# Kernel tuning notes

Measured on AMD Instinct MI355X. Metric: run time of the kernel, lower is better.

## Reference

```python
import jax, jax.numpy as jnp
import numpy as np

VOCAB, HIDDEN, EMBED = 30522, 768, 512
PAD_INDEX = 0
NEG_SLOPE = 0.1


def setup_inputs() -> dict:
    key = jax.random.key(0)
    k1, k2, k3, k4 = jax.random.split(key, 4)
    words = jax.random.randint(k1, (16, 512, 4), 0, VOCAB, dtype=jnp.int64) if jax.config.jax_enable_x64 else jax.random.randint(k1, (16, 512, 4), 0, VOCAB, dtype=jnp.int32)
    embed_table = jax.random.normal(k2, (VOCAB, HIDDEN), dtype=jnp.float32) * 0.02
    w_ffn = jax.random.normal(k3, (HIDDEN, EMBED), dtype=jnp.float32) * 0.02
    b_ffn = jax.random.normal(k4, (EMBED,), dtype=jnp.float32) * 0.02
    return {"words": words, "embed_table": embed_table, "w_ffn": w_ffn, "b_ffn": b_ffn}


def reference(words, embed_table, w_ffn, b_ffn):
    # words: [B, S, W] subword ids; pad_index marks padding subwords/words.
    B, S, W = words.shape
    sub_mask = words != PAD_INDEX                      # [B,S,W] valid subwords
    word_valid = jnp.any(sub_mask, axis=-1)            # [B,S]  words with >=1 subword
    lens = jnp.sum(word_valid, axis=-1)                # [B]    valid words per sequence

    # Stub of transformer last_hidden_state: per-token hidden vectors. [B,S,W,H]
    x = embed_table[words]

    # Masked mean over subwords of each word (segment mean-pool).
    m = sub_mask[..., None].astype(x.dtype)
    cnt = jnp.maximum(jnp.sum(sub_mask, axis=-1), 1)[..., None].astype(x.dtype)
    pooled = jnp.sum(x * m, axis=2) / cnt              # [B,S,H]

    # pad = x[0, -1] of flattened [B, S*W, H] == hidden of last flat token of batch 0
    pad_vec = x[0, -1, -1]                             # [H]

    # Stable compaction: valid words first (mirrors pop-in-order + pad append).
    order = jnp.argsort(jnp.logical_not(word_valid), axis=1, stable=True)  # [B,S]
    pooled_c = jnp.take_along_axis(pooled, order[..., None], axis=1)       # [B,S,H]
    keep = (jnp.arange(S)[None, :] < lens[:, None])[..., None]             # [B,S,1]
    x_seq = jnp.where(keep, pooled_c, pad_vec)         # [B,S,H]

    # FFN: Linear + LeakyReLU(0.1)
    return jax.nn.leaky_relu(x_seq @ w_ffn + b_ffn, NEG_SLOPE)
```

## Files before the change

kernel.cpp:

```cpp
#include <hip/hip_runtime.h>
#include <stdint.h>

#define HIDDEN 768
#define EMBED  512
#define BATCH  16
#define SEQ    512
#define NWORDS (BATCH*SEQ)
#define PAD_FLAT_IDX 2047
#define NEG_SLOPE 0.1f
#define SA_LD 776
#define BM 32

__device__ __forceinline__ unsigned short f2bf(float f) {
    unsigned int x = __float_as_uint(f);
    unsigned int r = x + 0x7fffu + ((x >> 16) & 1u);
    return (unsigned short)(r >> 16);
}

__global__ __launch_bounds__(256) void prep_kernel(const int* __restrict__ words,
                                                   const float* __restrict__ w,
                                                   int4* __restrict__ ids4,
                                                   int* __restrict__ cnts,
                                                   unsigned short* __restrict__ wt) {
    if (blockIdx.x < BATCH) {
        int b = blockIdx.x;
        int t = threadIdx.x;
        int s0 = 2 * t, s1 = 2 * t + 1;
        int4 wa = ((const int4*)words)[b * SEQ + s0];
        int4 wb = ((const int4*)words)[b * SEQ + s1];
        bool v0 = (wa.x | wa.y | wa.z | wa.w) != 0;
        bool v1 = (wb.x | wb.y | wb.z | wb.w) != 0;

        unsigned long long m0 = __ballot(v0);
        unsigned long long m1 = __ballot(v1);
        int lane = t & 63;
        int wave = t >> 6;
        unsigned long long below = (1ull << lane) - 1ull;
        int pre = __popcll(m0 & below) + __popcll(m1 & below);
        __shared__ int wsum[4];
        if (lane == 0) wsum[wave] = __popcll(m0) + __popcll(m1);
        __syncthreads();
        int off = 0, tot = 0;
#pragma unroll
        for (int i = 0; i < 4; ++i) {
            int x = wsum[i];
            if (i < wave) off += x;
            tot += x;
        }
        int vp0 = off + pre;
        int vp1 = vp0 + (v0 ? 1 : 0);
        int d0 = v0 ? vp0 : (tot + (s0 - vp0));
        int d1 = v1 ? vp1 : (tot + (s1 - vp1));

        int pid = words[PAD_FLAT_IDX];

        {
            int id[4] = {wa.x, wa.y, wa.z, wa.w};
            int o[4] = {0, 0, 0, 0};
            int c = 0;
#pragma unroll
            for (int j = 0; j < 4; ++j) if (id[j] != 0) o[c++] = id[j];
            if (c == 0) { o[0] = pid; c = 1; }
            ids4[b * SEQ + d0] = make_int4(o[0], o[1], o[2], o[3]);
            cnts[b * SEQ + d0] = c;
        }
        {
            int id[4] = {wb.x, wb.y, wb.z, wb.w};
            int o[4] = {0, 0, 0, 0};
            int c = 0;
#pragma unroll
            for (int j = 0; j < 4; ++j) if (id[j] != 0) o[c++] = id[j];
            if (c == 0) { o[0] = pid; c = 1; }
            ids4[b * SEQ + d1] = make_int4(o[0], o[1], o[2], o[3]);
            cnts[b * SEQ + d1] = c;
        }
    } else {
        __shared__ float tile[32][33];
        int bid = blockIdx.x - BATCH;
        int k0 = (bid % (HIDDEN / 32)) * 32;
        int n0 = (bid / (HIDDEN / 32)) * 32;
        int tc = threadIdx.x & 31;
        int tr = threadIdx.x >> 5;
#pragma unroll
        for (int i = 0; i < 4; ++i) {
            int r = tr + i * 8;
            tile[r][tc] = w[(size_t)(k0 + r) * EMBED + n0 + tc];
        }
        __syncthreads();
#pragma unroll
        for (int i = 0; i < 4; ++i) {
            int r = tr + i * 8;
            wt[(size_t)(n0 + r) * HIDDEN + k0 + tc] = f2bf(tile[tc][r]);
        }
    }
}

typedef __attribute__((ext_vector_type(8))) short bf16x8;
typedef __attribute__((ext_vector_type(4))) float f32x4;

__device__ __forceinline__ void load_lds16(const void* g, void* l) {
    __builtin_amdgcn_global_load_lds(
        (const __attribute__((address_space(1))) unsigned int*)g,
        (__attribute__((address_space(3))) unsigned int*)l,
        16, 0, 0);
}

__global__ __launch_bounds__(256) void fused_kernel(const int4* __restrict__ ids4,
                                                    const int* __restrict__ cnts,
                                                    const float* __restrict__ table,
                                                    const unsigned short* __restrict__ Bt,
                                                    const float* __restrict__ bias,
                                                    float* __restrict__ out) {
    __shared__ unsigned short sA[BM * SA_LD];
    __shared__ unsigned short sB[512 * 32];

    int tid  = threadIdx.x;
    int wave = tid >> 6;
    int lane = tid & 63;
    int m0   = blockIdx.x * BM;

#pragma unroll 2
    for (int i = 0; i < 8; ++i) {
        int rl  = i * 4 + wave;
        int row = m0 + rl;
        int4 w4 = ids4[row];
        int cnt = cnts[row];
        int id[4] = {w4.x, w4.y, w4.z, w4.w};
        float sx[3] = {0.f, 0.f, 0.f}, sy[3] = {0.f, 0.f, 0.f};
        float sz[3] = {0.f, 0.f, 0.f}, sw[3] = {0.f, 0.f, 0.f};
#pragma unroll
        for (int j = 0; j < 4; ++j) {
            if (j < cnt) {
                const float4* rp = (const float4*)(table + (size_t)id[j] * HIDDEN);
#pragma unroll
                for (int c = 0; c < 3; ++c) {
                    float4 v = rp[lane + 64 * c];
                    sx[c] += v.x; sy[c] += v.y; sz[c] += v.z; sw[c] += v.w;
                }
            }
        }
        float inv = 1.0f / (float)cnt;
#pragma unroll
        for (int c = 0; c < 3; ++c) {
            ushort4 o;
            o.x = f2bf(sx[c] * inv); o.y = f2bf(sy[c] * inv);
            o.z = f2bf(sz[c] * inv); o.w = f2bf(sw[c] * inv);
            *(ushort4*)&sA[rl * SA_LD + (lane + 64 * c) * 4] = o;
        }
    }

    int quad = lane >> 4;
    int l16  = lane & 15;
    f32x4 acc[2][8] = {};

    const unsigned short* gb = Bt + (size_t)(tid >> 2) * HIDDEN + (tid & 3) * 8;

    for (int k0 = 0; k0 < HIDDEN; k0 += 32) {
#pragma unroll
        for (int j = 0; j < 8; ++j)
            load_lds16(gb + (size_t)j * 64 * HIDDEN + k0, &sB[(tid + 256 * j) * 8]);
        __syncthreads();

        bf16x8 af[2], bfr[8];
#pragma unroll
        for (int mt = 0; mt < 2; ++mt)
            af[mt] = *(const bf16x8*)&sA[(mt * 16 + l16) * SA_LD + k0 + quad * 8];
#pragma unroll
        for (int nt = 0; nt < 8; ++nt)
            bfr[nt] = *(const bf16x8*)&sB[(wave * 128 + nt * 16 + l16) * 32 + quad * 8];

#pragma unroll
        for (int mt = 0; mt < 2; ++mt)
#pragma unroll
            for (int nt = 0; nt < 8; ++nt)
                acc[mt][nt] = __builtin_amdgcn_mfma_f32_16x16x32_bf16(
                    af[mt], bfr[nt], acc[mt][nt], 0, 0, 0);
        __syncthreads();
    }

#pragma unroll
    for (int nt = 0; nt < 8; ++nt) {
        int col = wave * 128 + nt * 16 + l16;
        float bv = bias[col];
#pragma unroll
        for (int mt = 0; mt < 2; ++mt) {
            int rbase = m0 + mt * 16 + quad * 4;
#pragma unroll
            for (int r = 0; r < 4; ++r) {
                float v = acc[mt][nt][r] + bv;
                v = (v > 0.f) ? v : v * NEG_SLOPE;
                out[(size_t)(rbase + r) * EMBED + col] = v;
            }
        }
    }
}

extern "C" void kernel_launch(void* const* d_in, const int* in_sizes, int n_in,
                              void* d_out, int out_size, void* d_ws, size_t ws_size,
                              hipStream_t stream) {
    (void)in_sizes; (void)n_in; (void)out_size; (void)ws_size;
    const int*   words = (const int*)d_in[0];
    const float* table = (const float*)d_in[1];
    const float* wffn  = (const float*)d_in[2];
    const float* bffn  = (const float*)d_in[3];
    float* out = (float*)d_out;

    char* ws = (char*)d_ws;
    unsigned short* wt   = (unsigned short*)ws;
    int4*           ids4 = (int4*)(ws + 786432);
    int*            cnts = (int*)(ws + 786432 + 131072);

    prep_kernel<<<BATCH + (HIDDEN / 32) * (EMBED / 32), 256, 0, stream>>>(
        words, wffn, ids4, cnts, wt);
    fused_kernel<<<NWORDS / BM, 256, 0, stream>>>(ids4, cnts, table, wt, bffn, out);
}
```

Before: 174.2 us.

## Split fused pool+GEMM into separate pool and tiled GEMM kernels with k-major layout

The fused kernel is split in two. A pooling kernel writes bf16 pooled rows to a global k-chunk-major buffer, and a separate GEMM kernel uses 128x64 tiles over a 2D grid, loading both operands via direct global-to-LDS copies in a k-major 8-element interleaved layout. The weight transpose now emits the same k-chunk layout. This aims to raise GEMM parallelism and reuse: 512 blocks instead of 256, and each block no longer streams the whole weight matrix per 32 rows. The cost is an extra 12MB intermediate round-trip through global memory and one more kernel launch.

```diff
diff --git a/kernel.cpp b/kernel.cpp
--- a/kernel.cpp
+++ b/kernel.cpp
@@ -6,10 +6,11 @@
 #define BATCH  16
 #define SEQ    512
 #define NWORDS (BATCH*SEQ)
+#define NKC    (HIDDEN/8)
 #define PAD_FLAT_IDX 2047
 #define NEG_SLOPE 0.1f
-#define SA_LD 776
-#define BM 32
+#define SP_LD 780
+
 
 __device__ __forceinline__ unsigned short f2bf(float f) {
     unsigned int x = __float_as_uint(f);
@@ -21,7 +22,7 @@
                                                    const float* __restrict__ w,
                                                    int4* __restrict__ ids4,
                                                    int* __restrict__ cnts,
-                                                   unsigned short* __restrict__ wt) {
+                                                   unsigned short* __restrict__ wtk) {
     if (blockIdx.x < BATCH) {
         int b = blockIdx.x;
         int t = threadIdx.x;
@@ -53,7 +54,6 @@
         int d1 = v1 ? vp1 : (tot + (s1 - vp1));
 
         int pid = words[PAD_FLAT_IDX];
-
         {
             int id[4] = {wa.x, wa.y, wa.z, wa.w};
             int o[4] = {0, 0, 0, 0};
@@ -87,37 +87,25 @@
             tile[r][tc] = w[(size_t)(k0 + r) * EMBED + n0 + tc];
         }
         __syncthreads();
+        int kc = (k0 >> 3) + (tc >> 3);
+        int ko = tc & 7;
 #pragma unroll
         for (int i = 0; i < 4; ++i) {
-            int r = tr + i * 8;
-            wt[(size_t)(n0 + r) * HIDDEN + k0 + tc] = f2bf(tile[tc][r]);
-        }
-    }
-}
-
-typedef __attribute__((ext_vector_type(8))) short bf16x8;
-typedef __attribute__((ext_vector_type(4))) float f32x4;
-
-__device__ __forceinline__ void load_lds16(const void* g, void* l) {
-    __builtin_amdgcn_global_load_lds(
-        (const __attribute__((address_space(1))) unsigned int*)g,
-        (__attribute__((address_space(3))) unsigned int*)l,
-        16, 0, 0);
-}
-
-__global__ __launch_bounds__(256) void fused_kernel(const int4* __restrict__ ids4,
-                                                    const int* __restrict__ cnts,
-                                                    const float* __restrict__ table,
-                                                    const unsigned short* __restrict__ Bt,
-                                                    const float* __restrict__ bias,
-                                                    float* __restrict__ out) {
-    __shared__ unsigned short sA[BM * SA_LD];
-    __shared__ unsigned short sB[512 * 32];
-
+            int n = n0 + tr + i * 8;
+            wtk[(size_t)kc * (EMBED * 8) + n * 8 + ko] = f2bf(tile[tc][n - n0]);
+        }
+    }
+}
+
+__global__ __launch_bounds__(256) void pool_kernel(const int4* __restrict__ ids4,
+                                                   const int* __restrict__ cnts,
+                                                   const float* __restrict__ table,
+                                                   unsigned short* __restrict__ xkm) {
+    __shared__ unsigned short sp[32 * SP_LD];
     int tid  = threadIdx.x;
     int wave = tid >> 6;
     int lane = tid & 63;
-    int m0   = blockIdx.x * BM;
+    int m0   = blockIdx.x * 32;
 
 #pragma unroll 2
     for (int i = 0; i < 8; ++i) {
@@ -145,46 +133,90 @@
             ushort4 o;
             o.x = f2bf(sx[c] * inv); o.y = f2bf(sy[c] * inv);
             o.z = f2bf(sz[c] * inv); o.w = f2bf(sw[c] * inv);
-            *(ushort4*)&sA[rl * SA_LD + (lane + 64 * c) * 4] = o;
-        }
-    }
-
+            *(ushort4*)&sp[rl * SP_LD + (lane + 64 * c) * 4] = o;
+        }
+    }
+    __syncthreads();
+
+    int rw = lane & 31;
+    int hf = lane >> 5;
+    for (int kc = wave; kc < NKC; kc += 4) {
+        ushort4 v = *(const ushort4*)&sp[rw * SP_LD + kc * 8 + hf * 4];
+        *(ushort4*)&xkm[(size_t)kc * (NWORDS * 8) + (m0 + rw) * 8 + hf * 4] = v;
+    }
+}
+
+typedef __attribute__((ext_vector_type(8))) short bf16x8;
+typedef __attribute__((ext_vector_type(4))) float f32x4;
+
+__device__ __forceinline__ void load_lds16(const void* g, void* l) {
+    __builtin_amdgcn_global_load_lds(
+        (const __attribute__((address_space(1))) unsigned int*)g,
+        (__attribute__((address_space(3))) unsigned int*)l,
+        16, 0, 0);
+}
+
+#define BM 128
+#define BN 64
+#define BK 32
+
+__global__ __launch_bounds__(256) void gemm_kernel(const unsigned short* __restrict__ xkm,
+                                                   const unsigned short* __restrict__ wtk,
+                                                   const float* __restrict__ bias,
+                                                   float* __restrict__ out) {
+    __shared__ unsigned short sA[4 * BM * 8];
+    __shared__ unsigned short sB[4 * BN * 8];
+
+    int tid  = threadIdx.x;
+    int m0   = blockIdx.x * BM;
+    int n0   = blockIdx.y * BN;
+    int wave = tid >> 6;
+    int lane = tid & 63;
+    int wr   = wave >> 1;
+    int wc   = wave & 1;
     int quad = lane >> 4;
     int l16  = lane & 15;
-    f32x4 acc[2][8] = {};
-
-    const unsigned short* gb = Bt + (size_t)(tid >> 2) * HIDDEN + (tid & 3) * 8;
-
-    for (int k0 = 0; k0 < HIDDEN; k0 += 32) {
-#pragma unroll
-        for (int j = 0; j < 8; ++j)
-            load_lds16(gb + (size_t)j * 64 * HIDDEN + k0, &sB[(tid + 256 * j) * 8]);
-        __syncthreads();
-
-        bf16x8 af[2], bfr[8];
-#pragma unroll
-        for (int mt = 0; mt < 2; ++mt)
-            af[mt] = *(const bf16x8*)&sA[(mt * 16 + l16) * SA_LD + k0 + quad * 8];
-#pragma unroll
-        for (int nt = 0; nt < 8; ++nt)
-            bfr[nt] = *(const bf16x8*)&sB[(wave * 128 + nt * 16 + l16) * 32 + quad * 8];
-
-#pragma unroll
-        for (int mt = 0; mt < 2; ++mt)
-#pragma unroll
-            for (int nt = 0; nt < 8; ++nt)
+
+    f32x4 acc[4][2] = {};
+
+    const unsigned short* gA0 = xkm + (size_t)(tid >> 7) * (NWORDS * 8) + (m0 + (tid & 127)) * 8;
+    const unsigned short* gA1 = xkm + (size_t)((tid + 256) >> 7) * (NWORDS * 8) + (m0 + ((tid + 256) & 127)) * 8;
+    const unsigned short* gB  = wtk + (size_t)(tid >> 6) * (EMBED * 8) + (n0 + (tid & 63)) * 8;
+
+    for (int k0 = 0; k0 < HIDDEN; k0 += BK) {
+        load_lds16(gA0 + (size_t)k0 * (NWORDS), &sA[tid * 8]);
+        load_lds16(gA1 + (size_t)k0 * (NWORDS), &sA[(256 + tid) * 8]);
+        load_lds16(gB  + (size_t)k0 * (EMBED),  &sB[tid * 8]);
+        __syncthreads();
+
+        bf16x8 af[4], bfr[2];
+#pragma unroll
+        for (int mt = 0; mt < 4; ++mt) {
+            int row_l = wr * 64 + mt * 16 + l16;
+            af[mt] = *(const bf16x8*)&sA[(quad * BM + row_l) * 8];
+        }
+#pragma unroll
+        for (int nt = 0; nt < 2; ++nt) {
+            int col_l = wc * 32 + nt * 16 + l16;
+            bfr[nt] = *(const bf16x8*)&sB[(quad * BN + col_l) * 8];
+        }
+
+#pragma unroll
+        for (int mt = 0; mt < 4; ++mt)
+#pragma unroll
+            for (int nt = 0; nt < 2; ++nt)
                 acc[mt][nt] = __builtin_amdgcn_mfma_f32_16x16x32_bf16(
                     af[mt], bfr[nt], acc[mt][nt], 0, 0, 0);
         __syncthreads();
     }
 
 #pragma unroll
-    for (int nt = 0; nt < 8; ++nt) {
-        int col = wave * 128 + nt * 16 + l16;
+    for (int nt = 0; nt < 2; ++nt) {
+        int col = n0 + wc * 32 + nt * 16 + l16;
         float bv = bias[col];
 #pragma unroll
-        for (int mt = 0; mt < 2; ++mt) {
-            int rbase = m0 + mt * 16 + quad * 4;
+        for (int mt = 0; mt < 4; ++mt) {
+            int rbase = m0 + wr * 64 + mt * 16 + quad * 4;
 #pragma unroll
             for (int r = 0; r < 4; ++r) {
                 float v = acc[mt][nt][r] + bv;
@@ -206,11 +238,13 @@
     float* out = (float*)d_out;
 
     char* ws = (char*)d_ws;
-    unsigned short* wt   = (unsigned short*)ws;
-    int4*           ids4 = (int4*)(ws + 786432);
-    int*            cnts = (int*)(ws + 786432 + 131072);
+    unsigned short* xkm  = (unsigned short*)ws;
+    unsigned short* wtk  = (unsigned short*)(ws + 12582912);
+    int4*           ids4 = (int4*)(ws + 12582912 + 786432);
+    int*            cnts = (int*)(ws + 12582912 + 786432 + 131072);
 
     prep_kernel<<<BATCH + (HIDDEN / 32) * (EMBED / 32), 256, 0, stream>>>(
-        words, wffn, ids4, cnts, wt);
-    fused_kernel<<<NWORDS / BM, 256, 0, stream>>>(ids4, cnts, table, wt, bffn, out);
-}
+        words, wffn, ids4, cnts, wtk);
+    pool_kernel<<<NWORDS / 32, 256, 0, stream>>>(ids4, cnts, table, xkm);
+    gemm_kernel<<<dim3(NWORDS / BM, EMBED / BN), 256, 0, stream>>>(xkm, wtk, bffn, out);
+}
```

Result: no change. 172.3 us (-1.1%).

## Stream gathered embedding rows per K-chunk and retile weights into k-chunk-major layout

Applied to the files above, without the earlier changes.

The up-front gather-and-pool of all 32 rows into a large LDS tile is replaced by per-K-step gathering: each K iteration loads 4 table float4s per thread, forms a weighted sum with precomputed 1/cnt weights, and writes a small bf16 A chunk into LDS alongside the B tile load. The transposed weight is stored in a k-chunk-major [K/8][N][8] layout so each B load is contiguous. Blocks grow to 512 threads (8 waves, each owning 64 columns), which shrinks LDS use and lets gather latency overlap with MFMA work. In exchange, table loads are issued as many small strided accesses across iterations, and half the threads sit idle during the gather.

```diff
diff --git a/kernel.cpp b/kernel.cpp
--- a/kernel.cpp
+++ b/kernel.cpp
@@ -6,10 +6,9 @@
 #define BATCH  16
 #define SEQ    512
 #define NWORDS (BATCH*SEQ)
+#define NKC    (HIDDEN/8)
 #define PAD_FLAT_IDX 2047
 #define NEG_SLOPE 0.1f
-#define SA_LD 776
-#define BM 32
 
 __device__ __forceinline__ unsigned short f2bf(float f) {
     unsigned int x = __float_as_uint(f);
@@ -21,7 +20,7 @@
                                                    const float* __restrict__ w,
                                                    int4* __restrict__ ids4,
                                                    int* __restrict__ cnts,
-                                                   unsigned short* __restrict__ wt) {
+                                                   unsigned short* __restrict__ wtk) {
     if (blockIdx.x < BATCH) {
         int b = blockIdx.x;
         int t = threadIdx.x;
@@ -53,7 +52,6 @@
         int d1 = v1 ? vp1 : (tot + (s1 - vp1));
 
         int pid = words[PAD_FLAT_IDX];
-
         {
             int id[4] = {wa.x, wa.y, wa.z, wa.w};
             int o[4] = {0, 0, 0, 0};
@@ -87,10 +85,12 @@
             tile[r][tc] = w[(size_t)(k0 + r) * EMBED + n0 + tc];
         }
         __syncthreads();
+        int kc = (k0 >> 3) + (tc >> 3);
+        int ko = tc & 7;
 #pragma unroll
         for (int i = 0; i < 4; ++i) {
-            int r = tr + i * 8;
-            wt[(size_t)(n0 + r) * HIDDEN + k0 + tc] = f2bf(tile[tc][r]);
+            int n = n0 + tr + i * 8;
+            wtk[(size_t)kc * (EMBED * 8) + n * 8 + ko] = f2bf(tile[tc][n - n0]);
         }
     }
 }
@@ -105,82 +105,84 @@
         16, 0, 0);
 }
 
-__global__ __launch_bounds__(256) void fused_kernel(const int4* __restrict__ ids4,
+__global__ __launch_bounds__(512) void fused_kernel(const int4* __restrict__ ids4,
                                                     const int* __restrict__ cnts,
                                                     const float* __restrict__ table,
-                                                    const unsigned short* __restrict__ Bt,
+                                                    const unsigned short* __restrict__ wtk,
                                                     const float* __restrict__ bias,
                                                     float* __restrict__ out) {
-    __shared__ unsigned short sA[BM * SA_LD];
-    __shared__ unsigned short sB[512 * 32];
+    __shared__ unsigned short sB[4 * EMBED * 8];
+    __shared__ unsigned short sA[4 * 32 * 8];
 
     int tid  = threadIdx.x;
     int wave = tid >> 6;
     int lane = tid & 63;
-    int m0   = blockIdx.x * BM;
-
-#pragma unroll 2
-    for (int i = 0; i < 8; ++i) {
-        int rl  = i * 4 + wave;
-        int row = m0 + rl;
-        int4 w4 = ids4[row];
-        int cnt = cnts[row];
-        int id[4] = {w4.x, w4.y, w4.z, w4.w};
-        float sx[3] = {0.f, 0.f, 0.f}, sy[3] = {0.f, 0.f, 0.f};
-        float sz[3] = {0.f, 0.f, 0.f}, sw[3] = {0.f, 0.f, 0.f};
-#pragma unroll
-        for (int j = 0; j < 4; ++j) {
-            if (j < cnt) {
-                const float4* rp = (const float4*)(table + (size_t)id[j] * HIDDEN);
-#pragma unroll
-                for (int c = 0; c < 3; ++c) {
-                    float4 v = rp[lane + 64 * c];
-                    sx[c] += v.x; sy[c] += v.y; sz[c] += v.z; sw[c] += v.w;
-                }
-            }
-        }
-        float inv = 1.0f / (float)cnt;
-#pragma unroll
-        for (int c = 0; c < 3; ++c) {
-            ushort4 o;
-            o.x = f2bf(sx[c] * inv); o.y = f2bf(sy[c] * inv);
-            o.z = f2bf(sz[c] * inv); o.w = f2bf(sw[c] * inv);
-            *(ushort4*)&sA[rl * SA_LD + (lane + 64 * c) * 4] = o;
-        }
-    }
-
     int quad = lane >> 4;
     int l16  = lane & 15;
-    f32x4 acc[2][8] = {};
-
-    const unsigned short* gb = Bt + (size_t)(tid >> 2) * HIDDEN + (tid & 3) * 8;
+    int m0   = blockIdx.x * 32;
+
+    int grow = tid >> 3;
+    int gl   = tid & 7;
+    const float* gp[4];
+    float gw[4];
+    {
+        int r = (tid < 256) ? (m0 + grow) : m0;
+        int4 w4 = ids4[r];
+        int cnt = cnts[r];
+        float inv = 1.0f / (float)cnt;
+        int idj[4] = {w4.x, w4.y, w4.z, w4.w};
+#pragma unroll
+        for (int j = 0; j < 4; ++j) {
+            gw[j] = (j < cnt) ? inv : 0.0f;
+            gp[j] = table + (size_t)idj[j] * HIDDEN + gl * 4;
+        }
+    }
+
+    f32x4 acc[2][4] = {};
 
     for (int k0 = 0; k0 < HIDDEN; k0 += 32) {
-#pragma unroll
-        for (int j = 0; j < 8; ++j)
-            load_lds16(gb + (size_t)j * 64 * HIDDEN + k0, &sB[(tid + 256 * j) * 8]);
-        __syncthreads();
-
-        bf16x8 af[2], bfr[8];
+        int kc0 = k0 >> 3;
+#pragma unroll
+        for (int j = 0; j < 4; ++j)
+            load_lds16(wtk + (size_t)(kc0 + j) * (EMBED * 8) + tid * 8,
+                       &sB[(j * EMBED + tid) * 8]);
+
+        if (tid < 256) {
+            float4 a = *(const float4*)(gp[0] + k0);
+            float4 b = *(const float4*)(gp[1] + k0);
+            float4 c = *(const float4*)(gp[2] + k0);
+            float4 d = *(const float4*)(gp[3] + k0);
+            float4 s;
+            s.x = gw[0] * a.x + gw[1] * b.x + gw[2] * c.x + gw[3] * d.x;
+            s.y = gw[0] * a.y + gw[1] * b.y + gw[2] * c.y + gw[3] * d.y;
+            s.z = gw[0] * a.z + gw[1] * b.z + gw[2] * c.z + gw[3] * d.z;
+            s.w = gw[0] * a.w + gw[1] * b.w + gw[2] * c.w + gw[3] * d.w;
+            ushort4 o;
+            o.x = f2bf(s.x); o.y = f2bf(s.y); o.z = f2bf(s.z); o.w = f2bf(s.w);
+            *(ushort4*)&sA[((gl >> 1) * 32 + grow) * 8 + (gl & 1) * 4] = o;
+        }
+        __syncthreads();
+
+        bf16x8 af[2], bfr[4];
 #pragma unroll
         for (int mt = 0; mt < 2; ++mt)
-            af[mt] = *(const bf16x8*)&sA[(mt * 16 + l16) * SA_LD + k0 + quad * 8];
-#pragma unroll
-        for (int nt = 0; nt < 8; ++nt)
-            bfr[nt] = *(const bf16x8*)&sB[(wave * 128 + nt * 16 + l16) * 32 + quad * 8];
+            af[mt] = *(const bf16x8*)&sA[(quad * 32 + mt * 16 + l16) * 8];
+#pragma unroll
+        for (int nt = 0; nt < 4; ++nt)
+            bfr[nt] = *(const bf16x8*)&sB[(quad * EMBED + wave * 64 + nt * 16 + l16) * 8];
 
 #pragma unroll
         for (int mt = 0; mt < 2; ++mt)
 #pragma unroll
-            for (int nt = 0; nt < 8; ++nt)
+            for (int nt = 0; nt < 4; ++nt)
                 acc[mt][nt] = __builtin_amdgcn_mfma_f32_16x16x32_bf16(
                     af[mt], bfr[nt], acc[mt][nt], 0, 0, 0);
         __syncthreads();
     }
 
 #pragma unroll
-    for (int nt = 0; nt < 8; ++nt) {
-        int col = wave * 128 + nt * 16 + l16;
+    for (int nt = 0; nt < 4; ++nt) {
+        int col = wave * 64 + nt * 16 + l16;
         float bv = bias[col];
 #pragma unroll
         for (int mt = 0; mt < 2; ++mt) {
@@ -206,11 +208,11 @@
     float* out = (float*)d_out;
 
     char* ws = (char*)d_ws;
-    unsigned short* wt   = (unsigned short*)ws;
+    unsigned short* wtk  = (unsigned short*)ws;
     int4*           ids4 = (int4*)(ws + 786432);
     int*            cnts = (int*)(ws + 786432 + 131072);
 
     prep_kernel<<<BATCH + (HIDDEN / 32) * (EMBED / 32), 256, 0, stream>>>(
-        words, wffn, ids4, cnts, wt);
-    fused_kernel<<<NWORDS / BM, 256, 0, stream>>>(ids4, cnts, table, wt, bffn, out);
-}
+        words, wffn, ids4, cnts, wtk);
+    fused_kernel<<<NWORDS / 32, 512, 0, stream>>>(ids4, cnts, table, wtk, bffn, out);
+}
```

After: 162.2 us. 1.07x faster.
